# Performance work log

Hardware: AMD Instinct MI355X
Metric: run time of the kernel (lower is better)

The kernel has to match this reference:

```python
import jax, jax.numpy as jnp
import numpy as np

HEADS = 16
MAX_SEQ_LEN = 1024
ALPHA = 1.0


def setup_inputs() -> dict:
    key = jax.random.key(0)
    ks = jax.random.split(key, 16)
    b, n, dim = 2, 1024, 1024
    s = 0.02
    x = jax.random.normal(ks[0], (b, n, dim), jnp.float32)
    Wq = jax.random.normal(ks[1], (dim, dim), jnp.float32) * s
    Wk = jax.random.normal(ks[2], (dim, dim), jnp.float32) * s
    Wv = jax.random.normal(ks[3], (dim, dim), jnp.float32) * s
    Wo = jax.random.normal(ks[4], (dim, dim), jnp.float32) * s
    E_idx = jax.random.normal(ks[5], (MAX_SEQ_LEN, HEADS), jnp.float32) * s
    # padding_idx=0 rows zero-initialized (as in torch nn.Embedding(padding_idx=0))
    E_bar = (jax.random.normal(ks[6], (17, HEADS), jnp.float32) * s).at[0].set(0.0)
    E_pos = (jax.random.normal(ks[7], (96, HEADS), jnp.float32) * s).at[0].set(0.0)
    E_oct = (jax.random.normal(ks[8], (25, HEADS), jnp.float32) * s).at[0].set(0.0)
    E_semi = (jax.random.normal(ks[9], (13, HEADS), jnp.float32) * s).at[0].set(0.0)
    # structure matrices: raw values in [0, table_size-2]; forward adds +1
    bar = jax.random.randint(ks[10], (b, n, n), 0, 16, dtype=jnp.int32)
    position = jax.random.randint(ks[11], (b, n, n), 0, 95, dtype=jnp.int32)
    octave = jax.random.randint(ks[12], (b, n, n), 0, 24, dtype=jnp.int32)
    semitone = jax.random.randint(ks[13], (b, n, n), 0, 12, dtype=jnp.int32)
    return {"x": x, "Wq": Wq, "Wk": Wk, "Wv": Wv, "Wo": Wo,
            "E_idx": E_idx, "E_bar": E_bar, "E_pos": E_pos,
            "E_oct": E_oct, "E_semi": E_semi,
            "bar": bar, "position": position, "octave": octave, "semitone": semitone}


def reference(x, Wq, Wk, Wv, Wo, E_idx, E_bar, E_pos, E_oct, E_semi,
              bar, position, octave, semitone):
    b, n, dim = x.shape
    h = HEADS
    d = dim // h

    def split_heads(t):  # (b,n,dim) -> (b,h,n,d)
        return t.reshape(b, n, h, d).transpose(0, 2, 1, 3)

    q = split_heads(x @ Wq.T)
    k = split_heads(x @ Wk.T)
    v = split_heads(x @ Wv.T)

    qk = jnp.einsum('bhid,bhjd->bhij', q, k)

    # relative index bias: (1,h,n,n)
    rel_pos = jnp.clip(jnp.arange(n)[:, None] - jnp.arange(n)[None, :], 0, MAX_SEQ_LEN - 1)
    srel = E_idx[rel_pos].transpose(2, 0, 1)[None]

    # structure biases: embedding lookups -> (b,h,n,n)
    s_time = (E_bar[bar + 1] + E_pos[position + 1]).transpose(0, 3, 1, 2)
    s_pitch = (E_oct[octave + 1] + E_semi[semitone + 1]).transpose(0, 3, 1, 2)

    dots = (qk + ALPHA * (srel + s_time + s_pitch)) / jnp.sqrt(jnp.float32(d))

    causal_mask = jnp.triu(jnp.ones((n, n), dtype=bool), k=1)
    mask_value = -jnp.finfo(dots.dtype).max
    dots = jnp.where(causal_mask, mask_value, dots)

    attn = jax.nn.softmax(dots, axis=-1)  # dropout=0 at eval
    out = jnp.einsum('bhij,bhjd->bhid', attn, v)
    out = out.transpose(0, 2, 1, 3).reshape(b, n, dim)
    return out @ Wo.T
```

## Files before the change

kernel.cpp:

```cpp
#include <hip/hip_runtime.h>
#include <cstdint>

typedef __attribute__((ext_vector_type(8))) short short8;
typedef __attribute__((ext_vector_type(4))) float f32x4;

#define LOG2E 1.44269504088896340736f

static __device__ __forceinline__ float bf2f(unsigned short u) {
    union { unsigned int i; float f; } v; v.i = ((unsigned int)u) << 16; return v.f;
}
static __device__ __forceinline__ unsigned short f2bf(float f) {
    union { float f; unsigned int i; } v; v.f = f;
    unsigned int r = v.i + 0x7FFF + ((v.i >> 16) & 1);
    return (unsigned short)(r >> 16);
}

__global__ __launch_bounds__(256) void k_convert(
    const float* __restrict__ x, const float* __restrict__ wq,
    const float* __restrict__ wk, const float* __restrict__ wv,
    const float* __restrict__ wo, unsigned short* __restrict__ dst) {
    long t = (long)blockIdx.x * 256 + threadIdx.x;
    long base = t * 4;
    const long NX = 2097152, NW = 1048576;
    const float* src; long off;
    if (base < NX)            { src = x;  off = base; }
    else if (base < NX + NW)  { src = wq; off = base - NX; }
    else if (base < NX + 2*NW){ src = wk; off = base - NX - NW; }
    else if (base < NX + 3*NW){ src = wv; off = base - NX - 2*NW; }
    else                      { src = wo; off = base - NX - 3*NW; }
    float4 v = *(const float4*)(src + off);
    ushort4 o;
    o.x = f2bf(v.x); o.y = f2bf(v.y); o.z = f2bf(v.z); o.w = f2bf(v.w);
    *(ushort4*)(dst + base) = o;
}

__global__ __launch_bounds__(256) void k_bias(
    const float* __restrict__ Eidx, const float* __restrict__ Ebar,
    const float* __restrict__ Epos, const float* __restrict__ Eoct,
    const float* __restrict__ Esemi,
    const int* __restrict__ barm, const int* __restrict__ posm,
    const int* __restrict__ octm, const int* __restrict__ semim,
    unsigned short* __restrict__ biasg) {
    int bid = blockIdx.x;
    int tj = bid & 15, ti = (bid >> 4) & 63, b = bid >> 10;
    int i0 = ti * 16, j0 = tj * 64;
    if (j0 > i0 + 15) return;

    __shared__ float lds_t[16 * 233];
    __shared__ int   pk[16 * 65];

    int t = threadIdx.x;
    int rel_lo = i0 - j0 - 63; if (rel_lo < 0) rel_lo = 0;

    for (int idx = t; idx < 231 * 16; idx += 256) {
        int s = idx >> 4, h = idx & 15;
        float v;
        if (s < 80) {
            int src = rel_lo + s; if (src > 1023) src = 1023;
            v = Eidx[src * 16 + h];
        } else if (s < 97)  v = Ebar[(s - 80) * 16 + h];
        else if (s < 193)   v = Epos[(s - 97) * 16 + h];
        else if (s < 218)   v = Eoct[(s - 193) * 16 + h];
        else                v = Esemi[(s - 218) * 16 + h];
        lds_t[h * 233 + s] = v;
    }
    #pragma unroll
    for (int cc = 0; cc < 4; cc++) {
        int cell = t + cc * 256;
        int i = i0 + (cell >> 6), j = j0 + (cell & 63);
        long ij = ((long)b << 20) + ((long)i << 10) + j;
        int v = (barm[ij] + 1) | ((posm[ij] + 1) << 5) |
                ((octm[ij] + 1) << 12) | ((semim[ij] + 1) << 17);
        pk[(cell >> 6) * 65 + (cell & 63)] = v;
    }
    __syncthreads();

    int h = t >> 4, r = t & 15;
    int i = i0 + r;
    int base_rel = i - j0 - rel_lo;
    const float* T = &lds_t[h * 233];
    unsigned short* dst = biasg +
        ((((long)(b * 16 + h) * 64 + ti) * 16 + tj) << 10) + (r >> 2) * 256 + (r & 3) * 4;
    #pragma unroll 4
    for (int a = 0; a < 16; a++) {
        ushort4 ov;
        #pragma unroll
        for (int jj = 0; jj < 4; jj++) {
            int col = a + 16 * jj;
            int p = pk[r * 65 + col];
            int sr = base_rel - col; if (sr < 0) sr = 0;
            float v = T[sr]
                    + T[80  + (p & 31)]
                    + T[97  + ((p >> 5)  & 127)]
                    + T[193 + ((p >> 12) & 31)]
                    + T[218 + ((p >> 17) & 15)];
            ((unsigned short*)&ov)[jj] = f2bf(v * 0.125f);
        }
        *(ushort4*)(dst + a * 16) = ov;
    }
}

__global__ __launch_bounds__(256) void k_gemm(
    const unsigned short* __restrict__ A,
    const unsigned short* __restrict__ B0, const unsigned short* __restrict__ B1,
    const unsigned short* __restrict__ B2,
    unsigned short* __restrict__ qd, unsigned short* __restrict__ kd,
    unsigned short* __restrict__ vtd, float* __restrict__ outf, int mode) {
    __shared__ unsigned short As[64][72];
    __shared__ unsigned short Bs[64][72];
    int md = (mode < 0) ? (int)blockIdx.z : mode;
    const unsigned short* B = (md == 1) ? B1 : (md == 2) ? B2 : B0;
    int m0 = blockIdx.x * 64, n0 = blockIdx.y * 64;
    int t = threadIdx.x;
    int w = t >> 6, lane = t & 63, g = lane >> 4, c = lane & 15;
    int srow = t >> 2, scg = t & 3;
    const int K = 1024;
    f32x4 zero = {0.f, 0.f, 0.f, 0.f};
    f32x4 acc[4];
    acc[0] = zero; acc[1] = zero; acc[2] = zero; acc[3] = zero;

    for (int k0 = 0; k0 < K; k0 += 64) {
        __syncthreads();
        *(short8*)&As[srow][scg * 16]     = *(const short8*)(A + (long)(m0 + srow) * K + k0 + scg * 16);
        *(short8*)&As[srow][scg * 16 + 8] = *(const short8*)(A + (long)(m0 + srow) * K + k0 + scg * 16 + 8);
        *(short8*)&Bs[srow][scg * 16]     = *(const short8*)(B + (long)(n0 + srow) * K + k0 + scg * 16);
        *(short8*)&Bs[srow][scg * 16 + 8] = *(const short8*)(B + (long)(n0 + srow) * K + k0 + scg * 16 + 8);
        __syncthreads();
        #pragma unroll
        for (int kk = 0; kk < 2; kk++) {
            short8 a = *(const short8*)&As[w * 16 + c][kk * 32 + g * 8];
            #pragma unroll
            for (int jc = 0; jc < 4; jc++) {
                short8 bf = *(const short8*)&Bs[jc * 16 + c][kk * 32 + g * 8];
                acc[jc] = __builtin_amdgcn_mfma_f32_16x16x32_bf16(a, bf, acc[jc], 0, 0, 0);
            }
        }
    }

    if (md <= 1) {
        unsigned short* dst = (md == 0) ? qd : kd;
        float scale = (md == 0) ? 0.125f : 1.0f;
        #pragma unroll
        for (int r = 0; r < 4; r++) {
            int mm = m0 + w * 16 + g * 4 + r;
            int bb = mm >> 10, ii = mm & 1023;
            #pragma unroll
            for (int jc = 0; jc < 4; jc++) {
                int nn = n0 + jc * 16 + c;
                int hh = nn >> 6, dd = nn & 63;
                dst[(((long)(bb * 16 + hh) << 10) + ii) * 64 + dd] = f2bf(acc[jc][r] * scale);
            }
        }
    } else if (md == 2) {
        int mm0 = m0 + w * 16 + g * 4;
        int bb = mm0 >> 10, ii = mm0 & 1023;
        #pragma unroll
        for (int jc = 0; jc < 4; jc++) {
            int nn = n0 + jc * 16 + c;
            int hh = nn >> 6, dd = nn & 63;
            ushort4 pkv;
            pkv.x = f2bf(acc[jc][0]); pkv.y = f2bf(acc[jc][1]);
            pkv.z = f2bf(acc[jc][2]); pkv.w = f2bf(acc[jc][3]);
            *(ushort4*)&vtd[(((long)(bb * 16 + hh) << 6) + dd) * 1024 + ii] = pkv;
        }
    } else {
        #pragma unroll
        for (int r = 0; r < 4; r++) {
            long mm = m0 + w * 16 + g * 4 + r;
            #pragma unroll
            for (int jc = 0; jc < 4; jc++) {
                int nn = n0 + jc * 16 + c;
                outf[mm * 1024 + nn] = acc[jc][r];
            }
        }
    }
}

__global__ __launch_bounds__(256) void k_attn(
    const unsigned short* __restrict__ Qs, const unsigned short* __restrict__ Ks,
    const unsigned short* __restrict__ VTs, const unsigned short* __restrict__ biasg,
    unsigned short* __restrict__ Os) {
    __shared__ char smem[4 * 5632];
    int bid = blockIdx.x;
    int it = 63 - (bid >> 5);
    int bh = bid & 31;
    int b = bh >> 4, h = bh & 15;
    int w = threadIdx.x >> 6;
    int lane = threadIdx.x & 63;
    int g = lane >> 4, c = lane & 15;
    int i0 = it * 16;

    char* wbase = smem + w * 5632;
    unsigned short* p_lds = (unsigned short*)wbase;

    long plane = ((long)bh) << 16;
    const unsigned short* Qp = Qs + plane;
    const unsigned short* Kp = Ks + plane;
    const unsigned short* Vp = VTs + plane;
    const unsigned short* Bt = biasg + (((long)bh * 64 + it) << 14);

    short8 q0 = *(const short8*)(Qp + (long)(i0 + c) * 64 + g * 8);
    short8 q1 = *(const short8*)(Qp + (long)(i0 + c) * 64 + 32 + g * 8);

    f32x4 zero = {0.f, 0.f, 0.f, 0.f};
    f32x4 o[4]; o[0] = zero; o[1] = zero; o[2] = zero; o[3] = zero;
    float l[4] = {0.f, 0.f, 0.f, 0.f};

    int nj = (it >> 2) + 1;
    for (int jt = w; jt < nj; jt += 4) {
        int j0 = jt * 64;
        f32x4 s[4]; s[0] = zero; s[1] = zero; s[2] = zero; s[3] = zero;
        #pragma unroll
        for (int jj = 0; jj < 4; jj++) {
            const unsigned short* kr = Kp + (long)(j0 + jj * 16 + c) * 64 + g * 8;
            short8 ka = *(const short8*)(kr);
            short8 kb = *(const short8*)(kr + 32);
            s[jj] = __builtin_amdgcn_mfma_f32_16x16x32_bf16(q0, ka, s[jj], 0, 0, 0);
            s[jj] = __builtin_amdgcn_mfma_f32_16x16x32_bf16(q1, kb, s[jj], 0, 0, 0);
        }
        const unsigned short* bp = Bt + (jt << 10) + lane * 16;
        short8 bv0 = *(const short8*)(bp);
        short8 bv1 = *(const short8*)(bp + 8);
        #pragma unroll
        for (int r = 0; r < 4; r++) {
            #pragma unroll
            for (int jj = 0; jj < 4; jj++) {
                int idx = r * 4 + jj;
                float bb = (idx < 8) ? bf2f((unsigned short)bv0[idx])
                                     : bf2f((unsigned short)bv1[idx - 8]);
                s[jj][r] += bb;
            }
        }
        if (jt == nj - 1) {
            #pragma unroll
            for (int r = 0; r < 4; r++) {
                int i = i0 + g * 4 + r;
                #pragma unroll
                for (int jj = 0; jj < 4; jj++) {
                    if (j0 + jj * 16 + c > i) s[jj][r] = -1e9f;
                }
            }
        }
        #pragma unroll
        for (int r = 0; r < 4; r++) {
            #pragma unroll
            for (int jj = 0; jj < 4; jj++) {
                float p = exp2f(__builtin_fmaf(s[jj][r], LOG2E, -8.0f * LOG2E));
                l[r] += p;
                union { float f; unsigned int u; } pu; pu.f = p;
                p_lds[(g * 4 + r) * 72 + c + 16 * jj] = (unsigned short)(pu.u >> 16);
            }
        }
        short8 pa0 = *(const short8*)&p_lds[c * 72 + g * 8];
        short8 pa1 = *(const short8*)&p_lds[c * 72 + 32 + g * 8];
        #pragma unroll
        for (int dd = 0; dd < 4; dd++) {
            const unsigned short* vb = Vp + (long)(dd * 16 + c) * 1024 + j0 + g * 8;
            short8 v0 = *(const short8*)(vb);
            short8 v1 = *(const short8*)(vb + 32);
            o[dd] = __builtin_amdgcn_mfma_f32_16x16x32_bf16(pa0, v0, o[dd], 0, 0, 0);
            o[dd] = __builtin_amdgcn_mfma_f32_16x16x32_bf16(pa1, v1, o[dd], 0, 0, 0);
        }
    }
    float* oc = (float*)wbase;
    float* lc = (float*)(wbase + 4352);
    #pragma unroll
    for (int dd = 0; dd < 4; dd++)
        #pragma unroll
        for (int r = 0; r < 4; r++)
            oc[lane * 17 + dd * 4 + r] = o[dd][r];
    #pragma unroll
    for (int r = 0; r < 4; r++) lc[lane * 5 + r] = l[r];
    __syncthreads();

    if (w == 0) {
        float linv[4];
        #pragma unroll
        for (int r = 0; r < 4; r++) {
            float lv = 0.f;
            #pragma unroll
            for (int ww = 0; ww < 4; ww++)
                lv += ((const float*)(smem + ww * 5632 + 4352))[lane * 5 + r];
            lv += __shfl_xor(lv, 1); lv += __shfl_xor(lv, 2);
            lv += __shfl_xor(lv, 4); lv += __shfl_xor(lv, 8);
            linv[r] = 1.0f / lv;
        }
        #pragma unroll
        for (int r = 0; r < 4; r++) {
            int i = i0 + g * 4 + r;
            unsigned short* op = Os + ((long)(b * 1024 + i)) * 1024 + h * 64;
            #pragma unroll
            for (int dd = 0; dd < 4; dd++) {
                float ov = 0.f;
                #pragma unroll
                for (int ww = 0; ww < 4; ww++)
                    ov += ((const float*)(smem + ww * 5632))[lane * 17 + dd * 4 + r];
                op[dd * 16 + c] = f2bf(ov * linv[r]);
            }
        }
    }
}

extern "C" void kernel_launch(void* const* d_in, const int* in_sizes, int n_in,
                              void* d_out, int out_size, void* d_ws, size_t ws_size,
                              hipStream_t stream) {
    const float* x     = (const float*)d_in[0];
    const float* Wq    = (const float*)d_in[1];
    const float* Wk    = (const float*)d_in[2];
    const float* Wv    = (const float*)d_in[3];
    const float* Wo    = (const float*)d_in[4];
    const float* Eidx  = (const float*)d_in[5];
    const float* Ebar  = (const float*)d_in[6];
    const float* Epos  = (const float*)d_in[7];
    const float* Eoct  = (const float*)d_in[8];
    const float* Esemi = (const float*)d_in[9];
    const int* barm    = (const int*)d_in[10];
    const int* posm    = (const int*)d_in[11];
    const int* octm    = (const int*)d_in[12];
    const int* semim   = (const int*)d_in[13];
    float* outf = (float*)d_out;

    unsigned short* w = (unsigned short*)d_ws;
    unsigned short* XB   = w;
    unsigned short* WQB  = w + 2097152;
    unsigned short* WKB  = w + 3145728;
    unsigned short* WVB  = w + 4194304;
    unsigned short* WOB  = w + 5242880;
    unsigned short* QS   = w + 6291456;
    unsigned short* KS   = w + 8388608;
    unsigned short* VTS  = w + 10485760;
    unsigned short* OS   = w + 12582912;
    unsigned short* BIAS = w + 14680064;

    k_convert<<<6144, 256, 0, stream>>>(x, Wq, Wk, Wv, Wo, w);
    k_bias<<<2048, 256, 0, stream>>>(Eidx, Ebar, Epos, Eoct, Esemi,
                                     barm, posm, octm, semim, BIAS);
    k_gemm<<<dim3(32, 16, 3), 256, 0, stream>>>(XB, WQB, WKB, WVB,
                                                QS, KS, VTS, nullptr, -1);
    k_attn<<<2048, 256, 0, stream>>>(QS, KS, VTS, BIAS, OS);
    k_gemm<<<dim3(32, 16, 1), 256, 0, stream>>>(OS, WOB, WOB, WOB,
                                                QS, KS, VTS, outf, 3);
}
```

Before: 123.9 us.

## Enlarge GEMM tiles to 128x128 with direct-to-LDS loads; compact causal bias grid

The projection GEMM now uses 128x128 output tiles, with each wave computing a 4x4 grid of MFMA fragments. Operands are staged with global_load_lds straight into unpadded LDS, which raises operand reuse per load and removes the register round trip. The bias kernel launches only the causal lower-triangle tiles via an index map instead of exiting empty blocks, and each thread computes two heads at once through float2 tables. Risks include LDS bank conflicts from dropping the padding, fewer GEMM blocks (384 for QKV, 128 for the output projection) leaving CUs underused, and higher register pressure.

Result: faster. 119.9 us (-3.2%).

```diff
diff --git a/kernel.cpp b/kernel.cpp
--- a/kernel.cpp
+++ b/kernel.cpp
@@ -1,5 +1,6 @@
 #include <hip/hip_runtime.h>
 #include <cstdint>
+#include <math.h>
 
 typedef __attribute__((ext_vector_type(8))) short short8;
 typedef __attribute__((ext_vector_type(4))) float f32x4;
@@ -41,28 +42,39 @@
     const int* __restrict__ barm, const int* __restrict__ posm,
     const int* __restrict__ octm, const int* __restrict__ semim,
     unsigned short* __restrict__ biasg) {
-    int bid = blockIdx.x;
-    int tj = bid & 15, ti = (bid >> 4) & 63, b = bid >> 10;
+    int fid = blockIdx.x;
+    int b = (fid >= 544) ? 1 : 0;
+    int f = fid - b * 544;
+    int ti, tj;
+    if (f >= 480) { int rr = f - 480; ti = 60 + (rr >> 4); tj = rr & 15; }
+    else {
+        int g = (int)(0.5f * (sqrtf(1.0f + 2.0f * (float)f) - 1.0f));
+        while (2 * (g + 1) * (g + 2) <= f) g++;
+        while (2 * g * (g + 1) > f) g--;
+        int rr = f - 2 * g * (g + 1);
+        int q = rr / (g + 1);
+        ti = g * 4 + q;
+        tj = rr - q * (g + 1);
+    }
     int i0 = ti * 16, j0 = tj * 64;
-    if (j0 > i0 + 15) return;
-
-    __shared__ float lds_t[16 * 233];
-    __shared__ int   pk[16 * 65];
+
+    __shared__ float2 t2[8 * 233];
+    __shared__ int    pk[16 * 65];
 
     int t = threadIdx.x;
     int rel_lo = i0 - j0 - 63; if (rel_lo < 0) rel_lo = 0;
 
-    for (int idx = t; idx < 231 * 16; idx += 256) {
-        int s = idx >> 4, h = idx & 15;
-        float v;
+    for (int idx = t; idx < 231 * 8; idx += 256) {
+        int s = idx >> 3, h2 = idx & 7;
+        float va, vb;
         if (s < 80) {
             int src = rel_lo + s; if (src > 1023) src = 1023;
-            v = Eidx[src * 16 + h];
-        } else if (s < 97)  v = Ebar[(s - 80) * 16 + h];
-        else if (s < 193)   v = Epos[(s - 97) * 16 + h];
-        else if (s < 218)   v = Eoct[(s - 193) * 16 + h];
-        else                v = Esemi[(s - 218) * 16 + h];
-        lds_t[h * 233 + s] = v;
+            va = Eidx[src * 16 + h2]; vb = Eidx[src * 16 + h2 + 8];
+        } else if (s < 97)  { va = Ebar[(s - 80) * 16 + h2];  vb = Ebar[(s - 80) * 16 + h2 + 8]; }
+        else if (s < 193)   { va = Epos[(s - 97) * 16 + h2];  vb = Epos[(s - 97) * 16 + h2 + 8]; }
+        else if (s < 218)   { va = Eoct[(s - 193) * 16 + h2]; vb = Eoct[(s - 193) * 16 + h2 + 8]; }
+        else                { va = Esemi[(s - 218) * 16 + h2]; vb = Esemi[(s - 218) * 16 + h2 + 8]; }
+        t2[h2 * 233 + s] = make_float2(va, vb);
     }
     #pragma unroll
     for (int cc = 0; cc < 4; cc++) {
@@ -75,28 +87,34 @@
     }
     __syncthreads();
 
-    int h = t >> 4, r = t & 15;
+    int r = t & 15, h2 = (t >> 4) & 7, ah = t >> 7;
     int i = i0 + r;
     int base_rel = i - j0 - rel_lo;
-    const float* T = &lds_t[h * 233];
-    unsigned short* dst = biasg +
-        ((((long)(b * 16 + h) * 64 + ti) * 16 + tj) << 10) + (r >> 2) * 256 + (r & 3) * 4;
+    const float2* T = &t2[h2 * 233];
+    long frag = (r >> 2) * 256 + (r & 3) * 4;
+    unsigned short* dstL = biasg + ((((long)(b * 16 + h2)     * 64 + ti) * 16 + tj) << 10) + frag;
+    unsigned short* dstH = biasg + ((((long)(b * 16 + h2 + 8) * 64 + ti) * 16 + tj) << 10) + frag;
     #pragma unroll 4
-    for (int a = 0; a < 16; a++) {
-        ushort4 ov;
+    for (int aa = 0; aa < 8; aa++) {
+        int a = ah * 8 + aa;
+        ushort4 ovL, ovH;
         #pragma unroll
         for (int jj = 0; jj < 4; jj++) {
             int col = a + 16 * jj;
             int p = pk[r * 65 + col];
             int sr = base_rel - col; if (sr < 0) sr = 0;
-            float v = T[sr]
-                    + T[80  + (p & 31)]
-                    + T[97  + ((p >> 5)  & 127)]
-                    + T[193 + ((p >> 12) & 31)]
-                    + T[218 + ((p >> 17) & 15)];
-            ((unsigned short*)&ov)[jj] = f2bf(v * 0.125f);
-        }
-        *(ushort4*)(dst + a * 16) = ov;
+            float2 v0 = T[sr];
+            float2 v1 = T[80  + (p & 31)];
+            float2 v2 = T[97  + ((p >> 5)  & 127)];
+            float2 v3 = T[193 + ((p >> 12) & 31)];
+            float2 v4 = T[218 + ((p >> 17) & 15)];
+            float xL = v0.x + v1.x + v2.x + v3.x + v4.x;
+            float xH = v0.y + v1.y + v2.y + v3.y + v4.y;
+            ((unsigned short*)&ovL)[jj] = f2bf(xL * 0.125f);
+            ((unsigned short*)&ovH)[jj] = f2bf(xH * 0.125f);
+        }
+        *(ushort4*)(dstL + a * 16) = ovL;
+        *(ushort4*)(dstH + a * 16) = ovH;
     }
 }
 
@@ -106,34 +124,53 @@
     const unsigned short* __restrict__ B2,
     unsigned short* __restrict__ qd, unsigned short* __restrict__ kd,
     unsigned short* __restrict__ vtd, float* __restrict__ outf, int mode) {
-    __shared__ unsigned short As[64][72];
-    __shared__ unsigned short Bs[64][72];
+    __shared__ unsigned short As[128 * 64];
+    __shared__ unsigned short Bs[128 * 64];
     int md = (mode < 0) ? (int)blockIdx.z : mode;
     const unsigned short* B = (md == 1) ? B1 : (md == 2) ? B2 : B0;
-    int m0 = blockIdx.x * 64, n0 = blockIdx.y * 64;
+    int m0 = blockIdx.x * 128, n0 = blockIdx.y * 128;
     int t = threadIdx.x;
     int w = t >> 6, lane = t & 63, g = lane >> 4, c = lane & 15;
-    int srow = t >> 2, scg = t & 3;
+    int wr = w >> 1, wc = w & 1;
     const int K = 1024;
     f32x4 zero = {0.f, 0.f, 0.f, 0.f};
-    f32x4 acc[4];
-    acc[0] = zero; acc[1] = zero; acc[2] = zero; acc[3] = zero;
-
+    f32x4 acc[4][4];
+    #pragma unroll
+    for (int m = 0; m < 4; m++)
+        #pragma unroll
+        for (int n = 0; n < 4; n++) acc[m][n] = zero;
+
+    int srow = w * 8 + (lane >> 3);
+    int scol = (lane & 7) * 8;
     for (int k0 = 0; k0 < K; k0 += 64) {
         __syncthreads();
-        *(short8*)&As[srow][scg * 16]     = *(const short8*)(A + (long)(m0 + srow) * K + k0 + scg * 16);
-        *(short8*)&As[srow][scg * 16 + 8] = *(const short8*)(A + (long)(m0 + srow) * K + k0 + scg * 16 + 8);
-        *(short8*)&Bs[srow][scg * 16]     = *(const short8*)(B + (long)(n0 + srow) * K + k0 + scg * 16);
-        *(short8*)&Bs[srow][scg * 16 + 8] = *(const short8*)(B + (long)(n0 + srow) * K + k0 + scg * 16 + 8);
+        #pragma unroll
+        for (int q = 0; q < 4; q++) {
+            int row = q * 32 + srow;
+            __builtin_amdgcn_global_load_lds(
+                (const __attribute__((address_space(1))) unsigned int*)(A + (long)(m0 + row) * K + k0 + scol),
+                (__attribute__((address_space(3))) unsigned int*)&As[(q * 32 + w * 8) * 64],
+                16, 0, 0);
+            __builtin_amdgcn_global_load_lds(
+                (const __attribute__((address_space(1))) unsigned int*)(B + (long)(n0 + row) * K + k0 + scol),
+                (__attribute__((address_space(3))) unsigned int*)&Bs[(q * 32 + w * 8) * 64],
+                16, 0, 0);
+        }
         __syncthreads();
         #pragma unroll
         for (int kk = 0; kk < 2; kk++) {
-            short8 a = *(const short8*)&As[w * 16 + c][kk * 32 + g * 8];
-            #pragma unroll
-            for (int jc = 0; jc < 4; jc++) {
-                short8 bf = *(const short8*)&Bs[jc * 16 + c][kk * 32 + g * 8];
-                acc[jc] = __builtin_amdgcn_mfma_f32_16x16x32_bf16(a, bf, acc[jc], 0, 0, 0);
-            }
+            short8 a[4], bb[4];
+            #pragma unroll
+            for (int m = 0; m < 4; m++)
+                a[m] = *(const short8*)&As[(wr * 64 + m * 16 + c) * 64 + kk * 32 + g * 8];
+            #pragma unroll
+            for (int n = 0; n < 4; n++)
+                bb[n] = *(const short8*)&Bs[(wc * 64 + n * 16 + c) * 64 + kk * 32 + g * 8];
+            #pragma unroll
+            for (int m = 0; m < 4; m++)
+                #pragma unroll
+                for (int n = 0; n < 4; n++)
+                    acc[m][n] = __builtin_amdgcn_mfma_f32_16x16x32_bf16(a[m], bb[n], acc[m][n], 0, 0, 0);
         }
     }
 
@@ -141,36 +178,45 @@
         unsigned short* dst = (md == 0) ? qd : kd;
         float scale = (md == 0) ? 0.125f : 1.0f;
         #pragma unroll
-        for (int r = 0; r < 4; r++) {
-            int mm = m0 + w * 16 + g * 4 + r;
-            int bb = mm >> 10, ii = mm & 1023;
-            #pragma unroll
-            for (int jc = 0; jc < 4; jc++) {
-                int nn = n0 + jc * 16 + c;
+        for (int m = 0; m < 4; m++) {
+            #pragma unroll
+            for (int r = 0; r < 4; r++) {
+                int mm = m0 + wr * 64 + m * 16 + g * 4 + r;
+                int bb2 = mm >> 10, ii = mm & 1023;
+                #pragma unroll
+                for (int n = 0; n < 4; n++) {
+                    int nn = n0 + wc * 64 + n * 16 + c;
+                    int hh = nn >> 6, dd = nn & 63;
+                    dst[(((long)(bb2 * 16 + hh) << 10) + ii) * 64 + dd] = f2bf(acc[m][n][r] * scale);
+                }
+            }
+        }
+    } else if (md == 2) {
+        #pragma unroll
+        for (int m = 0; m < 4; m++) {
+            int mm0 = m0 + wr * 64 + m * 16 + g * 4;
+            int bb2 = mm0 >> 10, ii = mm0 & 1023;
+            #pragma unroll
+            for (int n = 0; n < 4; n++) {
+                int nn = n0 + wc * 64 + n * 16 + c;
                 int hh = nn >> 6, dd = nn & 63;
-                dst[(((long)(bb * 16 + hh) << 10) + ii) * 64 + dd] = f2bf(acc[jc][r] * scale);
-            }
-        }
-    } else if (md == 2) {
-        int mm0 = m0 + w * 16 + g * 4;
-        int bb = mm0 >> 10, ii = mm0 & 1023;
-        #pragma unroll
-        for (int jc = 0; jc < 4; jc++) {
-            int nn = n0 + jc * 16 + c;
-            int hh = nn >> 6, dd = nn & 63;
-            ushort4 pkv;
-            pkv.x = f2bf(acc[jc][0]); pkv.y = f2bf(acc[jc][1]);
-            pkv.z = f2bf(acc[jc][2]); pkv.w = f2bf(acc[jc][3]);
-            *(ushort4*)&vtd[(((long)(bb * 16 + hh) << 6) + dd) * 1024 + ii] = pkv;
+                ushort4 pkv;
+                pkv.x = f2bf(acc[m][n][0]); pkv.y = f2bf(acc[m][n][1]);
+                pkv.z = f2bf(acc[m][n][2]); pkv.w = f2bf(acc[m][n][3]);
+                *(ushort4*)&vtd[(((long)(bb2 * 16 + hh) << 6) + dd) * 1024 + ii] = pkv;
+            }
         }
     } else {
         #pragma unroll
-        for (int r = 0; r < 4; r++) {
-            long mm = m0 + w * 16 + g * 4 + r;
-            #pragma unroll
-            for (int jc = 0; jc < 4; jc++) {
-                int nn = n0 + jc * 16 + c;
-                outf[mm * 1024 + nn] = acc[jc][r];
+        for (int m = 0; m < 4; m++) {
+            #pragma unroll
+            for (int r = 0; r < 4; r++) {
+                long mm = m0 + wr * 64 + m * 16 + g * 4 + r;
+                #pragma unroll
+                for (int n = 0; n < 4; n++) {
+                    int nn = n0 + wc * 64 + n * 16 + c;
+                    outf[mm * 1024 + nn] = acc[m][n][r];
+                }
             }
         }
     }
@@ -333,11 +379,11 @@
     unsigned short* BIAS = w + 14680064;
 
     k_convert<<<6144, 256, 0, stream>>>(x, Wq, Wk, Wv, Wo, w);
-    k_bias<<<2048, 256, 0, stream>>>(Eidx, Ebar, Epos, Eoct, Esemi,
+    k_bias<<<1088, 256, 0, stream>>>(Eidx, Ebar, Epos, Eoct, Esemi,
                                      barm, posm, octm, semim, BIAS);
-    k_gemm<<<dim3(32, 16, 3), 256, 0, stream>>>(XB, WQB, WKB, WVB,
-                                                QS, KS, VTS, nullptr, -1);
+    k_gemm<<<dim3(16, 8, 3), 256, 0, stream>>>(XB, WQB, WKB, WVB,
+                                               QS, KS, VTS, nullptr, -1);
     k_attn<<<2048, 256, 0, stream>>>(QS, KS, VTS, BIAS, OS);
-    k_gemm<<<dim3(32, 16, 1), 256, 0, stream>>>(OS, WOB, WOB, WOB,
-                                                QS, KS, VTS, outf, 3);
-}
+    k_gemm<<<dim3(16, 8, 1), 256, 0, stream>>>(OS, WOB, WOB, WOB,
+                                               QS, KS, VTS, outf, 3);
+}
```
